# Optimization experiments

Hardware: AMD Instinct MI355X
Metric: run time of the kernel (lower is better)

Reference implementation:

```python
import jax, jax.numpy as jnp
import numpy as np

B, N, C = 4, 8192, 128
NPOINT, NSAMPLE = 2048, 32
RADIUS = 0.1
EPS = 1e-5  # BatchNorm eps (eval mode with running stats)


def setup_inputs() -> dict:
    key = jax.random.key(0)
    k1, k2, k3 = jax.random.split(key, 3)
    return {
        "points_coor": jax.random.uniform(k1, (B, 3, N), dtype=jnp.float32),
        "points_fea": jax.random.normal(k2, (B, C, N), dtype=jnp.float32),
        "W": jax.random.normal(k3, (2 * C, C + 3), dtype=jnp.float32) * 0.05,
        "b": jnp.zeros((2 * C,), jnp.float32),
        "gamma": jnp.ones((2 * C,), jnp.float32),
        "beta": jnp.zeros((2 * C,), jnp.float32),
        "bn_mean": jnp.zeros((2 * C,), jnp.float32),
        "bn_var": jnp.ones((2 * C,), jnp.float32),
    }


def _fps_single(xyz):
    """Farthest point sampling for one cloud. xyz: (N,3) -> (NPOINT,) int32.
    Deterministic start at index 0 (torch version starts at a random index)."""
    n = xyz.shape[0]

    def body(carry, _):
        dist, farthest = carry
        centroid = xyz[farthest]                      # (3,)
        d = jnp.sum((xyz - centroid) ** 2, axis=-1)   # (N,)
        dist = jnp.minimum(dist, d)
        nxt = jnp.argmax(dist).astype(jnp.int32)
        return (dist, nxt), farthest

    init = (jnp.full((n,), 1e10, xyz.dtype), jnp.int32(0))
    (_, _), idx = jax.lax.scan(body, init, None, length=NPOINT)
    return idx


def _gather(points, idx):
    # points: (B,N,D), idx: (B,S,K) -> (B,S,K,D)
    return jax.vmap(lambda p, i: p[i])(points, idx)


def reference(points_coor, points_fea, W, b, gamma, beta, bn_mean, bn_var):
    coor = points_coor.transpose(0, 2, 1)  # (B,N,3)
    fea = points_fea.transpose(0, 2, 1)    # (B,N,C)

    # S: farthest point sampling
    fps_idx = jax.vmap(_fps_single)(coor)                              # (B,S)
    new_coor = jnp.take_along_axis(coor, fps_idx[:, :, None], axis=1)  # (B,S,3)

    # G: hybrid knn/ball query -- k nearest, out-of-radius replaced by nearest
    sq = (jnp.sum(new_coor ** 2, -1)[:, :, None]
          + jnp.sum(coor ** 2, -1)[:, None, :]
          - 2.0 * jnp.einsum('bsd,bnd->bsn', new_coor, coor))           # (B,S,N)
    neg_d, idx = jax.lax.top_k(-sq, NSAMPLE)                            # k smallest
    d = -neg_d
    group_idx = jnp.where(d > RADIUS ** 2, idx[:, :, 0:1], idx)         # (B,S,K)

    g_coor = (_gather(coor, group_idx) - new_coor[:, :, None, :]) / RADIUS  # (B,S,K,3)
    g_fea = _gather(fea, group_idx)                                         # (B,S,K,C)
    g = jnp.concatenate([g_fea, g_coor], axis=-1)                           # (B,S,K,C+3)

    # P: shared 1x1 conv + BN(eval) + ReLU, then max-pool over neighbors
    h = jnp.einsum('bskc,dc->bskd', g, W) + b
    h = gamma * (h - bn_mean) * jax.lax.rsqrt(bn_var + EPS) + beta
    h = jax.nn.relu(h)
    new_fea = jnp.max(h, axis=2)  # (B,S,2C)

    return new_coor.transpose(0, 2, 1), new_fea.transpose(0, 2, 1)
```

## Files before the change

kernel.cpp:

```cpp
#include <hip/hip_runtime.h>
#include <stdint.h>


typedef unsigned short u16;
typedef unsigned long long u64;
typedef __bf16 bf16x8 __attribute__((ext_vector_type(8)));
typedef float f32x4 __attribute__((ext_vector_type(4)));
typedef float f32x2 __attribute__((ext_vector_type(2)));

#define NB 4
#define NPTS 8192
#define CH 128
#define SPTS 2048
#define KN 32
#define CINP 160

__device__ __forceinline__ u16 f2b(float f) {
    unsigned x = __float_as_uint(f);
    unsigned r = (x + 0x7fffu + ((x >> 16) & 1u)) >> 16;
    return (u16)r;
}
__device__ __forceinline__ u64 umin64(u64 a, u64 b) { return a < b ? a : b; }

template <int CTRL>
__device__ __forceinline__ u64 dpp_max64(u64 k) {
    unsigned lo = (unsigned)k, hi = (unsigned)(k >> 32);
    unsigned mlo = (unsigned)__builtin_amdgcn_update_dpp((int)lo, (int)lo, CTRL, 0xF, 0xF, false);
    unsigned mhi = (unsigned)__builtin_amdgcn_update_dpp((int)hi, (int)hi, CTRL, 0xF, 0xF, false);
    u64 m = ((u64)mhi << 32) | mlo;
    return m > k ? m : k;
}
template <int CTRL>
__device__ __forceinline__ unsigned dpp_maxu(unsigned v) {
    unsigned mv = (unsigned)__builtin_amdgcn_update_dpp((int)v, (int)v, CTRL, 0xF, 0xF, false);
    return mv > v ? mv : v;
}

__global__ __launch_bounds__(256) void ktrans(const float* __restrict__ fea,
                                              u16* __restrict__ feaT) {
    __shared__ u16 T[128][130];
    int blk = blockIdx.x;
    int b = blk >> 6, nt = blk & 63;
    int n0 = nt * 128;
    int t = threadIdx.x;
#pragma unroll 4
    for (int it = 0; it < 64; ++it) {
        int idx = it * 256 + t;
        int c = idx >> 7, nl = idx & 127;
        T[nl][c] = f2b(fea[((size_t)(b * CH + c)) * NPTS + n0 + nl]);
    }
    __syncthreads();
#pragma unroll 4
    for (int it = 0; it < 64; ++it) {
        int idx = it * 256 + t;
        int nl = idx >> 7, c = idx & 127;
        feaT[((size_t)(b * NPTS + n0 + nl)) * CH + c] = T[nl][c];
    }
}

__global__ __launch_bounds__(256) void kmisc(const float* __restrict__ coor,
                                             const float* __restrict__ W,
                                             float* __restrict__ pp,
                                             u16* __restrict__ Wpad) {
    int gid = blockIdx.x * 256 + threadIdx.x;
    if (blockIdx.x < 128) {
        int n = gid & 8191, b = gid >> 13;
        const float* cb = coor + b * 3 * NPTS;
        float x = cb[n], y = cb[NPTS + n], z = cb[2 * NPTS + n];
        pp[gid] = __fadd_rn(__fadd_rn(__fmul_rn(x, x), __fmul_rn(y, y)),
                            __fmul_rn(z, z));
    } else {
        int i = gid - 128 * 256;
        if (i < 256 * CINP) {
            int d = i / CINP, k = i - d * CINP;
            Wpad[i] = (k < 131) ? f2b(W[d * 131 + k]) : (u16)0;
        }
    }
}

__global__ __launch_bounds__(256) void ksort(const float* __restrict__ coor,
                                             float* __restrict__ sxg,
                                             float* __restrict__ syg,
                                             float* __restrict__ szg,
                                             int* __restrict__ sog) {
    __shared__ int hist[16], base[16];
    int b = blockIdx.x, tid = threadIdx.x;
    const float* cb = coor + b * 3 * NPTS;
    if (tid < 16) hist[tid] = 0;
    __syncthreads();
    int bins[32];
#pragma unroll 4
    for (int i = 0; i < 32; ++i) {
        int n = tid * 32 + i;
        float x = cb[n], y = cb[NPTS + n];
        int bx = min(3, (int)(x * 4.0f));
        int by = min(3, (int)(y * 4.0f));
        int bin = by * 4 + bx;
        bins[i] = bin;
        atomicAdd(&hist[bin], 1);
    }
    __syncthreads();
    if (tid == 0) {
        int acc = 0;
        for (int k2 = 0; k2 < 16; ++k2) { base[k2] = acc; acc += hist[k2]; hist[k2] = 0; }
    }
    __syncthreads();
#pragma unroll 4
    for (int i = 0; i < 32; ++i) {
        int n = tid * 32 + i;
        int bin = bins[i];
        int pos = base[bin] + atomicAdd(&hist[bin], 1);
        sxg[b * NPTS + pos] = cb[n];
        syg[b * NPTS + pos] = cb[NPTS + n];
        szg[b * NPTS + pos] = cb[2 * NPTS + n];
        sog[b * NPTS + pos] = n;
    }
}

__global__ __launch_bounds__(1024) void kfps(const float* __restrict__ sxg,
                                             const float* __restrict__ syg,
                                             const float* __restrict__ szg,
                                             const int* __restrict__ sog,
                                             int* __restrict__ fpsIdx,
                                             float* __restrict__ outCoor) {
    __shared__ float4 sp[NPTS];
    __shared__ unsigned sWin[SPTS];
    __shared__ u64 sAtom[4];
    __shared__ int slot0s;
    int tid = threadIdx.x;
    int b = blockIdx.x;
    int lane = tid & 63;
    const float* gx = sxg + b * NPTS;
    const float* gy = syg + b * NPTS;
    const float* gz = szg + b * NPTS;
    const int* go = sog + b * NPTS;
    f32x2 X2[4], Y2[4], Z2[4], D2[4];
    unsigned PK[8];
    int n0 = tid * 8;
    if (tid < 4) sAtom[tid] = 0;
#pragma unroll
    for (int j = 0; j < 8; ++j) {
        float x = gx[n0 + j], y = gy[n0 + j], z = gz[n0 + j];
        sp[n0 + j] = make_float4(x, y, z, 0.0f);
        X2[j >> 1][j & 1] = x; Y2[j >> 1][j & 1] = y; Z2[j >> 1][j & 1] = z;
        D2[j >> 1][j & 1] = 1e10f;
        int oi = go[n0 + j];
        PK[j] = ((unsigned)oi << 16) | (unsigned)(n0 + j);
        if (oi == 0) slot0s = n0 + j;
    }
    float lox = X2[0][0], hix = lox, loy = Y2[0][0], hiy = loy, loz = Z2[0][0], hiz = loz;
#pragma unroll
    for (int j = 1; j < 8; ++j) {
        float x = X2[j >> 1][j & 1], y = Y2[j >> 1][j & 1], z = Z2[j >> 1][j & 1];
        lox = fminf(lox, x); hix = fmaxf(hix, x);
        loy = fminf(loy, y); hiy = fmaxf(hiy, y);
        loz = fminf(loz, z); hiz = fmaxf(hiz, z);
    }
#pragma unroll
    for (int off = 32; off > 0; off >>= 1) {
        lox = fminf(lox, __shfl_xor(lox, off)); hix = fmaxf(hix, __shfl_xor(hix, off));
        loy = fminf(loy, __shfl_xor(loy, off)); hiy = fmaxf(hiy, __shfl_xor(hiy, off));
        loz = fminf(loz, __shfl_xor(loz, off)); hiz = fmaxf(hiz, __shfl_xor(hiz, off));
    }
    __syncthreads();
    int far = slot0s;
    if (tid == 0) sWin[0] = (unsigned)slot0s;
    float wMaxF = 3.4e38f;
    u64 cachedKey = 1;
    for (int t = 1; t < SPTS; ++t) {
        float4 c = sp[far];
        float fx = c.x, fy = c.y, fz = c.z;
        float ddx = fmaxf(0.0f, fmaxf(lox - fx, fx - hix));
        float ddy = fmaxf(0.0f, fmaxf(loy - fy, fy - hiy));
        float ddz = fmaxf(0.0f, fmaxf(loz - fz, fz - hiz));
        float dmin2 = ddx * ddx + ddy * ddy + ddz * ddz;
        if (!(dmin2 * 0.9995f >= wMaxF)) {
            {
#pragma clang fp contract(off)
                f32x2 fx2 = {fx, fx}, fy2 = {fy, fy}, fz2 = {fz, fz};
#pragma unroll
                for (int i = 0; i < 4; ++i) {
                    f32x2 dx = X2[i] - fx2;
                    f32x2 dy = Y2[i] - fy2;
                    f32x2 dz = Z2[i] - fz2;
                    f32x2 s = (dx * dx + dy * dy) + dz * dz;
                    D2[i][0] = fminf(D2[i][0], s[0]);
                    D2[i][1] = fminf(D2[i][1], s[1]);
                }
            }
            float m01 = fmaxf(D2[0][0], D2[0][1]), m23 = fmaxf(D2[1][0], D2[1][1]);
            float m45 = fmaxf(D2[2][0], D2[2][1]), m67 = fmaxf(D2[3][0], D2[3][1]);
            float m = fmaxf(fmaxf(m01, m23), fmaxf(m45, m67));
            unsigned sel = 0xFFFFFFFFu;
#pragma unroll
            for (int j = 0; j < 8; ++j) {
                float dj = D2[j >> 1][j & 1];
                sel = (dj == m) ? (sel < PK[j] ? sel : PK[j]) : sel;
            }
            unsigned mbits = __float_as_uint(m);
            unsigned r = mbits;
            r = dpp_maxu<0xB1>(r);
            r = dpp_maxu<0x4E>(r);
            r = dpp_maxu<0x141>(r);
            r = dpp_maxu<0x140>(r);
            r = dpp_maxu<0x142>(r);
            r = dpp_maxu<0x143>(r);
            unsigned wmaxb = (unsigned)__builtin_amdgcn_readlane((int)r, 63);
            u64 ball = __ballot(mbits == wmaxb);
            unsigned wpk;
            if (__popcll(ball) == 1) {
                int l = __ffsll(ball) - 1;
                wpk = (unsigned)__builtin_amdgcn_readlane((int)sel, l);
            } else {
                u64 kk = (mbits == wmaxb) ? (((u64)wmaxb << 32) | (unsigned)~sel) : 0ull;
                kk = dpp_max64<0xB1>(kk);
                kk = dpp_max64<0x4E>(kk);
                kk = dpp_max64<0x141>(kk);
                kk = dpp_max64<0x140>(kk);
                kk = dpp_max64<0x142>(kk);
                kk = dpp_max64<0x143>(kk);
                unsigned lo = (unsigned)__builtin_amdgcn_readlane((int)(unsigned)kk, 63);
                wpk = ~lo;
            }
            cachedKey = ((u64)wmaxb << 32) | (unsigned)~wpk;
            wMaxF = __uint_as_float(wmaxb);
        }
        if (lane == 63) atomicMax(&sAtom[t & 3], cachedKey);
        if (tid == 0) sAtom[(t + 1) & 3] = 0;
        __syncthreads();
        u64 wk = sAtom[t & 3];
        unsigned pk = ~(unsigned)wk;
        far = (int)(pk & 0xFFFFu);
        if (tid == 0) sWin[t] = pk;
    }
    __syncthreads();
    for (int i = tid; i < SPTS; i += 1024) {
        unsigned pk = sWin[i];
        int slot = (int)(pk & 0xFFFFu);
        float4 c = sp[slot];
        fpsIdx[b * SPTS + i] = (int)(pk >> 16);
        float* oc = outCoor + b * 3 * SPTS + i;
        oc[0] = c.x; oc[SPTS] = c.y; oc[2 * SPTS] = c.z;
    }
}

__global__ __launch_bounds__(256) void kgroup(const float* __restrict__ coor,
                                              const float* __restrict__ pp,
                                              const int* __restrict__ fpsIdx,
                                              int* __restrict__ gidxOut) {
    __shared__ u64 buf[4][256];
    __shared__ int cnt[4];
    int tid = threadIdx.x;
    int wv = tid >> 6, lane = tid & 63;
    if (tid < 4) cnt[tid] = 0;
    __syncthreads();
    int row = blockIdx.x * 4 + wv;
    int b = row >> 11, s = row & 2047;
    const float* cb = coor + b * 3 * NPTS;
    int n0 = fpsIdx[b * SPTS + s];
    float cx = cb[n0], cy = cb[NPTS + n0], cz = cb[2 * NPTS + n0];
    float cc = __fadd_rn(__fadd_rn(__fmul_rn(cx, cx), __fmul_rn(cy, cy)),
                         __fmul_rn(cz, cz));
    const float* ppb = pp + b * NPTS;
    u64 mk = ~0ull;
    for (int n = lane; n < NPTS; n += 64) {
        float x = cb[n], y = cb[NPTS + n], z = cb[2 * NPTS + n];
        float dot = __fmaf_rn(cz, z, __fmaf_rn(cy, y, __fmul_rn(cx, x)));
        float sq = __fsub_rn(__fadd_rn(cc, ppb[n]), __fmul_rn(2.0f, dot));
        unsigned ub = __float_as_uint(sq);
        ub ^= (ub >> 31) ? 0xFFFFFFFFu : 0x80000000u;
        u64 key = ((u64)ub << 32) | (unsigned)n;
        mk = umin64(mk, key);
        if (sq <= 0.01f) {
            int p = atomicAdd(&cnt[wv], 1);
            if (p < 256) buf[wv][p] = key;
        }
    }
#pragma unroll
    for (int off = 32; off > 0; off >>= 1) mk = umin64(mk, __shfl_xor(mk, off));
    int C = cnt[wv];
    if (C > 256) C = 256;
    int* go = gidxOut + row * KN;
    if (C <= 32) {
        if (lane < 32) {
            unsigned idx = (lane < C) ? (unsigned)buf[wv][lane] : (unsigned)mk;
            go[lane] = (int)idx;
        }
    } else {
        u64 e[4];
#pragma unroll
        for (int i = 0; i < 4; ++i) {
            int j2 = lane + (i << 6);
            e[i] = (j2 < C) ? buf[wv][j2] : ~0ull;
        }
        int cl = 0;
        unsigned sel = 0;
        for (int it = 0; it < 32; ++it) {
            u64 lb = ~0ull;
            int li = 0;
#pragma unroll
            for (int i = 0; i < 4; ++i) {
                bool f = (((cl >> i) & 1) == 0) && (e[i] < lb);
                lb = f ? e[i] : lb;
                li = f ? i : li;
            }
            u64 wmin = lb;
#pragma unroll
            for (int off = 32; off > 0; off >>= 1) wmin = umin64(wmin, __shfl_xor(wmin, off));
            u64 bal = __ballot(lb == wmin);
            int src = __ffsll((unsigned long long)bal) - 1;
            if (lane == src) cl |= (1 << li);
            if (lane == it) sel = (unsigned)wmin;
        }
        if (lane < 32) go[lane] = (int)sel;
    }
}

__global__ __launch_bounds__(256) void kfeat(const float* __restrict__ coor,
                                             const u16* __restrict__ feaT,
                                             const u16* __restrict__ Wpad,
                                             const float* __restrict__ bias,
                                             const float* __restrict__ gamma,
                                             const float* __restrict__ beta,
                                             const float* __restrict__ bmean,
                                             const float* __restrict__ bvar,
                                             const int* __restrict__ fpsIdx,
                                             const int* __restrict__ gidx,
                                             float* __restrict__ outFea) {
    __shared__ u16 g[KN][168];
    int row = blockIdx.x;
    int b = row >> 11, s = row & 2047;
    int tid = threadIdx.x;
    {
        int k = tid >> 3, j = tid & 7;
        const float* cb = coor + b * 3 * NPTS;
        int nc = fpsIdx[b * SPTS + s];
        int nbr = gidx[row * KN + k];
        const uint4* f4 = (const uint4*)(feaT + (((size_t)b * NPTS + nbr) << 7));
        uint4* gr = (uint4*)&g[k][0];
        gr[j] = f4[j];
        gr[j + 8] = f4[j + 8];
        for (int c = 128 + j; c < CINP; c += 8) {
            u16 v = 0;
            if (c < 131) {
                int dim = c - 128;
                float pv = cb[dim * NPTS + nbr];
                float cv = cb[dim * NPTS + nc];
                v = f2b(__fdiv_rn(__fsub_rn(pv, cv), 0.1f));
            }
            g[k][c] = v;
        }
    }
    __syncthreads();
    int w = tid >> 6, lane = tid & 63;
    int mrow = lane & 15, q = lane >> 4;
    f32x4 acc[4][2] = {};
#pragma unroll
    for (int ks = 0; ks < 5; ++ks) {
        int kb = ks * 32 + q * 8;
        bf16x8 b0 = *(const bf16x8*)&g[mrow][kb];
        bf16x8 b1 = *(const bf16x8*)&g[mrow + 16][kb];
#pragma unroll
        for (int mt = 0; mt < 4; ++mt) {
            bf16x8 a = *(const bf16x8*)&Wpad[(size_t)(w * 64 + mt * 16 + mrow) * CINP + kb];
            acc[mt][0] = __builtin_amdgcn_mfma_f32_16x16x32_bf16(a, b0, acc[mt][0], 0, 0, 0);
            acc[mt][1] = __builtin_amdgcn_mfma_f32_16x16x32_bf16(a, b1, acc[mt][1], 0, 0, 0);
        }
    }
#pragma unroll
    for (int mt = 0; mt < 4; ++mt) {
#pragma unroll
        for (int r = 0; r < 4; ++r) {
            int m = w * 64 + mt * 16 + q * 4 + r;
            float ga = gamma[m], be = beta[m];
            float mu = bmean[m], va = bvar[m], bi = bias[m];
            float rs = 1.0f / sqrtf(va + 1e-5f);
            float h0 = acc[mt][0][r] + bi;
            h0 = fmaxf(ga * (h0 - mu) * rs + be, 0.0f);
            float h1 = acc[mt][1][r] + bi;
            h1 = fmaxf(ga * (h1 - mu) * rs + be, 0.0f);
            float v = fmaxf(h0, h1);
#pragma unroll
            for (int off = 1; off < 16; off <<= 1) v = fmaxf(v, __shfl_xor(v, off));
            if (mrow == 0) outFea[((size_t)(b * 256 + m)) * SPTS + s] = v;
        }
    }
}

extern "C" void kernel_launch(void* const* d_in, const int* in_sizes, int n_in,
                              void* d_out, int out_size, void* d_ws, size_t ws_size,
                              hipStream_t stream) {
    const float* coor = (const float*)d_in[0];
    const float* fea = (const float*)d_in[1];
    const float* W = (const float*)d_in[2];
    const float* bias = (const float*)d_in[3];
    const float* gamma = (const float*)d_in[4];
    const float* beta = (const float*)d_in[5];
    const float* bmean = (const float*)d_in[6];
    const float* bvar = (const float*)d_in[7];
    char* ws = (char*)d_ws;
    int* fpsIdx = (int*)ws;
    int* gidx = (int*)(ws + 32768);
    float* pp = (float*)(ws + 32768 + 1048576);
    u16* feaT = (u16*)(ws + 1212416);
    u16* Wpad = (u16*)(ws + 9601024);
    float* sxg = (float*)(ws + 9682944);
    float* syg = (float*)(ws + 9814016);
    float* szg = (float*)(ws + 9945088);
    int* sog = (int*)(ws + 10076160);
    float* outC = (float*)d_out;
    float* outF = outC + NB * 3 * SPTS;

    ktrans<<<256, 256, 0, stream>>>(fea, feaT);
    kmisc<<<288, 256, 0, stream>>>(coor, W, pp, Wpad);
    ksort<<<NB, 256, 0, stream>>>(coor, sxg, syg, szg, sog);
    kfps<<<NB, 1024, 0, stream>>>(sxg, syg, szg, sog, fpsIdx, outC);
    kgroup<<<2048, 256, 0, stream>>>(coor, pp, fpsIdx, gidx);
    kfeat<<<8192, 256, 0, stream>>>(coor, feaT, Wpad, bias, gamma, beta, bmean, bvar,
                                    fpsIdx, gidx, outF);
}
```

Before: 1.815 ms.

## Replace FPS atomicMax barrier reduction with per-wave key slots and broadcast coords

In the farthest-point-sampling loop, each wave's winning lane now writes its key and the winning point's coordinates to a double-buffered per-wave shared slot, replacing the shared atomicMax. After the barrier, every wave reduces the 16 keys with DPP max and takes the winning coordinates by shuffle. This removes the atomic, the per-iteration reset and the dependent LDS load of the centroid from the serial critical path. In exchange it adds extra LDS traffic, and it relies on slot>>9 naming the owning wave and on cached keys staying valid when a wave skips its update.

```diff
diff --git a/kernel.cpp b/kernel.cpp
--- a/kernel.cpp
+++ b/kernel.cpp
@@ -125,11 +125,13 @@
                                              float* __restrict__ outCoor) {
     __shared__ float4 sp[NPTS];
     __shared__ unsigned sWin[SPTS];
-    __shared__ u64 sAtom[4];
+    __shared__ u64 sKeys[2][16];
+    __shared__ float4 sCoords[2][16];
     __shared__ int slot0s;
     int tid = threadIdx.x;
     int b = blockIdx.x;
     int lane = tid & 63;
+    int wv = tid >> 6;
     const float* gx = sxg + b * NPTS;
     const float* gy = syg + b * NPTS;
     const float* gz = szg + b * NPTS;
@@ -137,7 +139,10 @@
     f32x2 X2[4], Y2[4], Z2[4], D2[4];
     unsigned PK[8];
     int n0 = tid * 8;
-    if (tid < 4) sAtom[tid] = 0;
+    if (tid < 32) {
+        sKeys[tid >> 4][tid & 15] = 0;
+        sCoords[tid >> 4][tid & 15] = make_float4(0.f, 0.f, 0.f, 0.f);
+    }
 #pragma unroll
     for (int j = 0; j < 8; ++j) {
         float x = gx[n0 + j], y = gy[n0 + j], z = gz[n0 + j];
@@ -163,13 +168,15 @@
         loz = fminf(loz, __shfl_xor(loz, off)); hiz = fmaxf(hiz, __shfl_xor(hiz, off));
     }
     __syncthreads();
-    int far = slot0s;
+    float4 c0 = sp[slot0s];
+    float fx = c0.x, fy = c0.y, fz = c0.z;
     if (tid == 0) sWin[0] = (unsigned)slot0s;
     float wMaxF = 3.4e38f;
-    u64 cachedKey = 1;
+    bool win = false;
+    u64 ckey = 0;
+    float bX = 0.f, bY = 0.f, bZ = 0.f;
+    int li = lane & 15;
     for (int t = 1; t < SPTS; ++t) {
-        float4 c = sp[far];
-        float fx = c.x, fy = c.y, fz = c.z;
         float ddx = fmaxf(0.0f, fmaxf(lox - fx, fx - hix));
         float ddy = fmaxf(0.0f, fmaxf(loy - fy, fy - hiy));
         float ddz = fmaxf(0.0f, fmaxf(loz - fz, fz - hiz));
@@ -207,10 +214,9 @@
             r = dpp_maxu<0x143>(r);
             unsigned wmaxb = (unsigned)__builtin_amdgcn_readlane((int)r, 63);
             u64 ball = __ballot(mbits == wmaxb);
-            unsigned wpk;
+            bool iw;
             if (__popcll(ball) == 1) {
-                int l = __ffsll(ball) - 1;
-                wpk = (unsigned)__builtin_amdgcn_readlane((int)sel, l);
+                iw = (mbits == wmaxb);
             } else {
                 u64 kk = (mbits == wmaxb) ? (((u64)wmaxb << 32) | (unsigned)~sel) : 0ull;
                 kk = dpp_max64<0xB1>(kk);
@@ -220,17 +226,38 @@
                 kk = dpp_max64<0x142>(kk);
                 kk = dpp_max64<0x143>(kk);
                 unsigned lo = (unsigned)__builtin_amdgcn_readlane((int)(unsigned)kk, 63);
-                wpk = ~lo;
-            }
-            cachedKey = ((u64)wmaxb << 32) | (unsigned)~wpk;
+                iw = (mbits == wmaxb) && ((unsigned)~sel == lo);
+            }
+            win = iw;
+            if (iw) {
+                ckey = ((u64)wmaxb << 32) | (unsigned)~sel;
+#pragma unroll
+                for (int j = 0; j < 8; ++j) {
+                    if (PK[j] == sel) {
+                        bX = X2[j >> 1][j & 1];
+                        bY = Y2[j >> 1][j & 1];
+                        bZ = Z2[j >> 1][j & 1];
+                    }
+                }
+            }
             wMaxF = __uint_as_float(wmaxb);
         }
-        if (lane == 63) atomicMax(&sAtom[t & 3], cachedKey);
-        if (tid == 0) sAtom[(t + 1) & 3] = 0;
+        if (win) {
+            sKeys[t & 1][wv] = ckey;
+            sCoords[t & 1][wv] = make_float4(bX, bY, bZ, 0.0f);
+        }
         __syncthreads();
-        u64 wk = sAtom[t & 3];
-        unsigned pk = ~(unsigned)wk;
-        far = (int)(pk & 0xFFFFu);
+        u64 k = sKeys[t & 1][li];
+        float4 c4 = sCoords[t & 1][li];
+        k = dpp_max64<0xB1>(k);
+        k = dpp_max64<0x4E>(k);
+        k = dpp_max64<0x141>(k);
+        k = dpp_max64<0x140>(k);
+        unsigned pk = ~(unsigned)k;
+        int wstar = (int)((pk & 0xFFFFu) >> 9);
+        fx = __shfl(c4.x, wstar);
+        fy = __shfl(c4.y, wstar);
+        fz = __shfl(c4.z, wstar);
         if (tid == 0) sWin[t] = pk;
     }
     __syncthreads();
```

Measured after the change: 2.213 ms. 21.9% more time.

## Broadcast FPS winner coordinates via per-wave candidate slots and skip redundant reductions

Applied to the files above, without the earlier changes.

Each wave's winning lane now writes its candidate point coordinates into a small shared array alongside the atomic key. After the barrier, every lane reads the 16 candidates and uses readlane to pick the winning wave's coordinates, replacing the dependent shared-memory load sp[far] on the serial critical path. A per-wave ballot also skips the whole max/argmax reduction when the wave's previous winner is still its maximum. Vector min/max builtins are used for the distance updates. This adds extra shared writes and bookkeeping per iteration, and the skip path depends on exact float equality to stay correct.

```diff
diff --git a/kernel.cpp b/kernel.cpp
--- a/kernel.cpp
+++ b/kernel.cpp
@@ -126,10 +126,13 @@
     __shared__ float4 sp[NPTS];
     __shared__ unsigned sWin[SPTS];
     __shared__ u64 sAtom[4];
+    __shared__ float4 sCand[2][16];
     __shared__ int slot0s;
     int tid = threadIdx.x;
     int b = blockIdx.x;
     int lane = tid & 63;
+    int wv = tid >> 6;
+    int li = lane & 15;
     const float* gx = sxg + b * NPTS;
     const float* gy = syg + b * NPTS;
     const float* gz = szg + b * NPTS;
@@ -138,6 +141,7 @@
     unsigned PK[8];
     int n0 = tid * 8;
     if (tid < 4) sAtom[tid] = 0;
+    if (tid < 32) sCand[tid >> 4][tid & 15] = make_float4(0.f, 0.f, 0.f, 0.f);
 #pragma unroll
     for (int j = 0; j < 8; ++j) {
         float x = gx[n0 + j], y = gy[n0 + j], z = gz[n0 + j];
@@ -163,18 +167,21 @@
         loz = fminf(loz, __shfl_xor(loz, off)); hiz = fmaxf(hiz, __shfl_xor(hiz, off));
     }
     __syncthreads();
-    int far = slot0s;
+    float4 c0 = sp[slot0s];
+    float fx = c0.x, fy = c0.y, fz = c0.z;
     if (tid == 0) sWin[0] = (unsigned)slot0s;
     float wMaxF = 3.4e38f;
     u64 cachedKey = 1;
+    bool win = false;
+    float bX = 0.f, bY = 0.f, bZ = 0.f;
+    float cvD = 3.4e38f;
     for (int t = 1; t < SPTS; ++t) {
-        float4 c = sp[far];
-        float fx = c.x, fy = c.y, fz = c.z;
         float ddx = fmaxf(0.0f, fmaxf(lox - fx, fx - hix));
         float ddy = fmaxf(0.0f, fmaxf(loy - fy, fy - hiy));
         float ddz = fmaxf(0.0f, fmaxf(loz - fz, fz - hiz));
         float dmin2 = ddx * ddx + ddy * ddy + ddz * ddz;
         if (!(dmin2 * 0.9995f >= wMaxF)) {
+            float sc;
             {
 #pragma clang fp contract(off)
                 f32x2 fx2 = {fx, fx}, fy2 = {fy, fy}, fz2 = {fz, fz};
@@ -184,53 +191,78 @@
                     f32x2 dy = Y2[i] - fy2;
                     f32x2 dz = Z2[i] - fz2;
                     f32x2 s = (dx * dx + dy * dy) + dz * dz;
-                    D2[i][0] = fminf(D2[i][0], s[0]);
-                    D2[i][1] = fminf(D2[i][1], s[1]);
+                    D2[i] = __builtin_elementwise_min(D2[i], s);
                 }
+                float cdx = bX - fx, cdy = bY - fy, cdz = bZ - fz;
+                sc = (cdx * cdx + cdy * cdy) + cdz * cdz;
             }
-            float m01 = fmaxf(D2[0][0], D2[0][1]), m23 = fmaxf(D2[1][0], D2[1][1]);
-            float m45 = fmaxf(D2[2][0], D2[2][1]), m67 = fmaxf(D2[3][0], D2[3][1]);
-            float m = fmaxf(fmaxf(m01, m23), fmaxf(m45, m67));
-            unsigned sel = 0xFFFFFFFFu;
-#pragma unroll
-            for (int j = 0; j < 8; ++j) {
-                float dj = D2[j >> 1][j & 1];
-                sel = (dj == m) ? (sel < PK[j] ? sel : PK[j]) : sel;
+            cvD = fminf(cvD, sc);
+            if (__ballot(win && (cvD == wMaxF)) == 0ull) {
+                f32x2 t01 = __builtin_elementwise_max(D2[0], D2[1]);
+                f32x2 t23 = __builtin_elementwise_max(D2[2], D2[3]);
+                f32x2 t03 = __builtin_elementwise_max(t01, t23);
+                float m = fmaxf(t03[0], t03[1]);
+                unsigned sel = 0xFFFFFFFFu;
+#pragma unroll
+                for (int j = 0; j < 8; ++j) {
+                    float dj = D2[j >> 1][j & 1];
+                    sel = (dj == m) ? (sel < PK[j] ? sel : PK[j]) : sel;
+                }
+                unsigned mbits = __float_as_uint(m);
+                unsigned r = mbits;
+                r = dpp_maxu<0xB1>(r);
+                r = dpp_maxu<0x4E>(r);
+                r = dpp_maxu<0x141>(r);
+                r = dpp_maxu<0x140>(r);
+                r = dpp_maxu<0x142>(r);
+                r = dpp_maxu<0x143>(r);
+                unsigned wmaxb = (unsigned)__builtin_amdgcn_readlane((int)r, 63);
+                u64 ball = __ballot(mbits == wmaxb);
+                unsigned wpk;
+                bool iw;
+                if (__popcll(ball) == 1) {
+                    int l = __ffsll(ball) - 1;
+                    wpk = (unsigned)__builtin_amdgcn_readlane((int)sel, l);
+                    iw = (mbits == wmaxb);
+                } else {
+                    u64 kk = (mbits == wmaxb) ? (((u64)wmaxb << 32) | (unsigned)~sel) : 0ull;
+                    kk = dpp_max64<0xB1>(kk);
+                    kk = dpp_max64<0x4E>(kk);
+                    kk = dpp_max64<0x141>(kk);
+                    kk = dpp_max64<0x140>(kk);
+                    kk = dpp_max64<0x142>(kk);
+                    kk = dpp_max64<0x143>(kk);
+                    unsigned lo = (unsigned)__builtin_amdgcn_readlane((int)(unsigned)kk, 63);
+                    wpk = ~lo;
+                    iw = (mbits == wmaxb) && ((unsigned)~sel == lo);
+                }
+                win = iw;
+                if (iw) {
+                    cvD = m;
+#pragma unroll
+                    for (int j = 0; j < 8; ++j) {
+                        if (PK[j] == sel) {
+                            bX = X2[j >> 1][j & 1];
+                            bY = Y2[j >> 1][j & 1];
+                            bZ = Z2[j >> 1][j & 1];
+                        }
+                    }
+                }
+                cachedKey = ((u64)wmaxb << 32) | (unsigned)~wpk;
+                wMaxF = __uint_as_float(wmaxb);
             }
-            unsigned mbits = __float_as_uint(m);
-            unsigned r = mbits;
-            r = dpp_maxu<0xB1>(r);
-            r = dpp_maxu<0x4E>(r);
-            r = dpp_maxu<0x141>(r);
-            r = dpp_maxu<0x140>(r);
-            r = dpp_maxu<0x142>(r);
-            r = dpp_maxu<0x143>(r);
-            unsigned wmaxb = (unsigned)__builtin_amdgcn_readlane((int)r, 63);
-            u64 ball = __ballot(mbits == wmaxb);
-            unsigned wpk;
-            if (__popcll(ball) == 1) {
-                int l = __ffsll(ball) - 1;
-                wpk = (unsigned)__builtin_amdgcn_readlane((int)sel, l);
-            } else {
-                u64 kk = (mbits == wmaxb) ? (((u64)wmaxb << 32) | (unsigned)~sel) : 0ull;
-                kk = dpp_max64<0xB1>(kk);
-                kk = dpp_max64<0x4E>(kk);
-                kk = dpp_max64<0x141>(kk);
-                kk = dpp_max64<0x140>(kk);
-                kk = dpp_max64<0x142>(kk);
-                kk = dpp_max64<0x143>(kk);
-                unsigned lo = (unsigned)__builtin_amdgcn_readlane((int)(unsigned)kk, 63);
-                wpk = ~lo;
-            }
-            cachedKey = ((u64)wmaxb << 32) | (unsigned)~wpk;
-            wMaxF = __uint_as_float(wmaxb);
         }
         if (lane == 63) atomicMax(&sAtom[t & 3], cachedKey);
+        if (win) sCand[t & 1][wv] = make_float4(bX, bY, bZ, 0.0f);
         if (tid == 0) sAtom[(t + 1) & 3] = 0;
         __syncthreads();
         u64 wk = sAtom[t & 3];
+        float4 c4 = sCand[t & 1][li];
         unsigned pk = ~(unsigned)wk;
-        far = (int)(pk & 0xFFFFu);
+        int wstar = (int)((pk & 0xFFFFu) >> 9);
+        fx = __uint_as_float((unsigned)__builtin_amdgcn_readlane((int)__float_as_uint(c4.x), wstar));
+        fy = __uint_as_float((unsigned)__builtin_amdgcn_readlane((int)__float_as_uint(c4.y), wstar));
+        fz = __uint_as_float((unsigned)__builtin_amdgcn_readlane((int)__float_as_uint(c4.z), wstar));
         if (tid == 0) sWin[t] = pk;
     }
     __syncthreads();
```

New measurement: 1.997 ms. 1.1x slower.

## Refine spatial sort with z-bins and use per-thread bounds for FPS pruning

Applied to the files above, without the earlier changes.

The spatial presort now bins points into 256 cells (4x4 in xy, 16 slabs in z) instead of 16 xy cells, so each thread's 8 contiguous points form a tighter box. The FPS kernel keeps per-thread bounding boxes and per-thread max distances instead of wave-wide ones, and a wave skips the update only when no lane could have changed. The per-lane min/max updates are also rewritten as packed 2-wide vector ops. The aim is to skip more distance updates per iteration. The cost is a longer serial prefix scan in the sort and a ballot on every iteration.

```diff
diff --git a/kernel.cpp b/kernel.cpp
--- a/kernel.cpp
+++ b/kernel.cpp
@@ -83,26 +83,27 @@
                                              float* __restrict__ syg,
                                              float* __restrict__ szg,
                                              int* __restrict__ sog) {
-    __shared__ int hist[16], base[16];
+    __shared__ int hist[256], base[256];
     int b = blockIdx.x, tid = threadIdx.x;
     const float* cb = coor + b * 3 * NPTS;
-    if (tid < 16) hist[tid] = 0;
+    hist[tid] = 0;
     __syncthreads();
     int bins[32];
 #pragma unroll 4
     for (int i = 0; i < 32; ++i) {
         int n = tid * 32 + i;
-        float x = cb[n], y = cb[NPTS + n];
+        float x = cb[n], y = cb[NPTS + n], z = cb[2 * NPTS + n];
         int bx = min(3, (int)(x * 4.0f));
         int by = min(3, (int)(y * 4.0f));
-        int bin = by * 4 + bx;
+        int bz = min(15, (int)(z * 16.0f));
+        int bin = ((by * 4 + bx) << 4) | bz;
         bins[i] = bin;
         atomicAdd(&hist[bin], 1);
     }
     __syncthreads();
     if (tid == 0) {
         int acc = 0;
-        for (int k2 = 0; k2 < 16; ++k2) { base[k2] = acc; acc += hist[k2]; hist[k2] = 0; }
+        for (int k2 = 0; k2 < 256; ++k2) { base[k2] = acc; acc += hist[k2]; hist[k2] = 0; }
     }
     __syncthreads();
 #pragma unroll 4
@@ -138,6 +139,7 @@
     unsigned PK[8];
     int n0 = tid * 8;
     if (tid < 4) sAtom[tid] = 0;
+    float lox, hix, loy, hiy, loz, hiz;
 #pragma unroll
     for (int j = 0; j < 8; ++j) {
         float x = gx[n0 + j], y = gy[n0 + j], z = gz[n0 + j];
@@ -147,25 +149,18 @@
         int oi = go[n0 + j];
         PK[j] = ((unsigned)oi << 16) | (unsigned)(n0 + j);
         if (oi == 0) slot0s = n0 + j;
-    }
-    float lox = X2[0][0], hix = lox, loy = Y2[0][0], hiy = loy, loz = Z2[0][0], hiz = loz;
-#pragma unroll
-    for (int j = 1; j < 8; ++j) {
-        float x = X2[j >> 1][j & 1], y = Y2[j >> 1][j & 1], z = Z2[j >> 1][j & 1];
-        lox = fminf(lox, x); hix = fmaxf(hix, x);
-        loy = fminf(loy, y); hiy = fmaxf(hiy, y);
-        loz = fminf(loz, z); hiz = fmaxf(hiz, z);
-    }
-#pragma unroll
-    for (int off = 32; off > 0; off >>= 1) {
-        lox = fminf(lox, __shfl_xor(lox, off)); hix = fmaxf(hix, __shfl_xor(hix, off));
-        loy = fminf(loy, __shfl_xor(loy, off)); hiy = fmaxf(hiy, __shfl_xor(hiy, off));
-        loz = fminf(loz, __shfl_xor(loz, off)); hiz = fmaxf(hiz, __shfl_xor(hiz, off));
+        if (j == 0) {
+            lox = hix = x; loy = hiy = y; loz = hiz = z;
+        } else {
+            lox = fminf(lox, x); hix = fmaxf(hix, x);
+            loy = fminf(loy, y); hiy = fmaxf(hiy, y);
+            loz = fminf(loz, z); hiz = fmaxf(hiz, z);
+        }
     }
     __syncthreads();
     int far = slot0s;
     if (tid == 0) sWin[0] = (unsigned)slot0s;
-    float wMaxF = 3.4e38f;
+    float lm = 3.4e38f;
     u64 cachedKey = 1;
     for (int t = 1; t < SPTS; ++t) {
         float4 c = sp[far];
@@ -174,7 +169,7 @@
         float ddy = fmaxf(0.0f, fmaxf(loy - fy, fy - hiy));
         float ddz = fmaxf(0.0f, fmaxf(loz - fz, fz - hiz));
         float dmin2 = ddx * ddx + ddy * ddy + ddz * ddz;
-        if (!(dmin2 * 0.9995f >= wMaxF)) {
+        if (__ballot(dmin2 * 0.9995f < lm) != 0ull) {
             {
 #pragma clang fp contract(off)
                 f32x2 fx2 = {fx, fx}, fy2 = {fy, fy}, fz2 = {fz, fz};
@@ -184,13 +179,14 @@
                     f32x2 dy = Y2[i] - fy2;
                     f32x2 dz = Z2[i] - fz2;
                     f32x2 s = (dx * dx + dy * dy) + dz * dz;
-                    D2[i][0] = fminf(D2[i][0], s[0]);
-                    D2[i][1] = fminf(D2[i][1], s[1]);
+                    D2[i] = __builtin_elementwise_min(D2[i], s);
                 }
             }
-            float m01 = fmaxf(D2[0][0], D2[0][1]), m23 = fmaxf(D2[1][0], D2[1][1]);
-            float m45 = fmaxf(D2[2][0], D2[2][1]), m67 = fmaxf(D2[3][0], D2[3][1]);
-            float m = fmaxf(fmaxf(m01, m23), fmaxf(m45, m67));
+            f32x2 t01 = __builtin_elementwise_max(D2[0], D2[1]);
+            f32x2 t23 = __builtin_elementwise_max(D2[2], D2[3]);
+            f32x2 t03 = __builtin_elementwise_max(t01, t23);
+            float m = fmaxf(t03[0], t03[1]);
+            lm = m;
             unsigned sel = 0xFFFFFFFFu;
 #pragma unroll
             for (int j = 0; j < 8; ++j) {
@@ -223,7 +219,6 @@
                 wpk = ~lo;
             }
             cachedKey = ((u64)wmaxb << 32) | (unsigned)~wpk;
-            wMaxF = __uint_as_float(wmaxb);
         }
         if (lane == 63) atomicMax(&sAtom[t & 3], cachedKey);
         if (tid == 0) sAtom[(t + 1) & 3] = 0;
```

Measured after the change: 1.647 ms. 1.1x faster.
